# Optimization experiments

Measured on AMD Instinct MI355X. Metric: run time of the kernel, lower is better.

Reference implementation:

```python
import jax, jax.numpy as jnp
import numpy as np

EPS = 1e-5

def _point_batch_norm(x, gamma, beta):
    # BatchNorm1d over channel dim of (B, N, C): stats over (B, N), biased var (training mode)
    mu = jnp.mean(x, axis=(0, 1))
    var = jnp.var(x, axis=(0, 1))
    return (x - mu) * jax.lax.rsqrt(var + EPS) * gamma + beta

def setup_inputs() -> dict:
    key = jax.random.key(0)
    ks = jax.random.split(key, 10)
    B, M, N, K = 4, 16384, 32768, 16
    C, Cs, O = 64, 64, 64
    curr_coords = jax.random.normal(ks[0], (B, M, 3), jnp.float32)
    curr_feat = jax.random.normal(ks[1], (B, M, C), jnp.float32)
    skip_coords = jax.random.normal(ks[2], (B, N, 3), jnp.float32)
    skip_feat = jax.random.normal(ks[3], (B, N, Cs), jnp.float32)
    upsampling_idxs = jax.random.randint(ks[4], (B, N, K), 0, M, jnp.int64)
    s1 = 1.0 / np.sqrt(C)
    s2 = 1.0 / np.sqrt(Cs)
    W1 = jax.random.uniform(ks[5], (C, O), jnp.float32, -s1, s1)
    b1 = jax.random.uniform(ks[6], (O,), jnp.float32, -s1, s1)
    W2 = jax.random.uniform(ks[7], (Cs, O), jnp.float32, -s2, s2)
    b2 = jax.random.uniform(ks[8], (O,), jnp.float32, -s2, s2)
    g1 = jnp.ones((O,), jnp.float32); beta1 = jnp.zeros((O,), jnp.float32)
    g2 = jnp.ones((O,), jnp.float32); beta2 = jnp.zeros((O,), jnp.float32)
    return {
        "curr_coords": curr_coords, "curr_feat": curr_feat,
        "skip_coords": skip_coords, "skip_feat": skip_feat,
        "upsampling_idxs": upsampling_idxs,
        "W1": W1, "b1": b1, "g1": g1, "beta1": beta1,
        "W2": W2, "b2": b2, "g2": g2, "beta2": beta2,
    }

def reference(curr_coords, curr_feat, skip_coords, skip_feat, upsampling_idxs,
              W1, b1, g1, beta1, W2, b2, g2, beta2):
    # Gather K-NN neighbor features per skip point: (B, N, K, C), then max over K
    gathered = jax.vmap(lambda f, i: f[i])(curr_feat, upsampling_idxs)
    pooled = jnp.max(gathered, axis=2)  # (B, N, C)
    # proj: Linear -> PointBatchNorm -> ReLU
    h = jax.nn.relu(_point_batch_norm(pooled @ W1 + b1, g1, beta1))
    # proj_skip on skip features
    hs = jax.nn.relu(_point_batch_norm(skip_feat @ W2 + b2, g2, beta2))
    return jnp.concatenate([skip_coords, h, hs], axis=-1)  # (B, N, 3 + 2*O)
```

## Files before the change

kernel.cpp:

```cpp
#include <hip/hip_runtime.h>
#include <hip/hip_bf16.h>

#define BB 4
#define MM 16384
#define NN 32768
#define KK 16
#define ROWS (BB * NN)
#define OUTW 131
#define RPW 32
#define A_BLOCKS (ROWS / (RPW * 4))

__global__ __launch_bounds__(256) void k_pool_proj(
    const float* __restrict__ cf, const int* __restrict__ idxs,
    const float* __restrict__ scoord,
    const float* __restrict__ W1, const float* __restrict__ b1,
    float* __restrict__ out, float* __restrict__ acc)
{
    __shared__ float pool[4][64];
    __shared__ float lsum[64], lsq[64];
    const int lane = threadIdx.x & 63;
    const int wv   = threadIdx.x >> 6;
    if (threadIdx.x < 64) { lsum[threadIdx.x] = 0.f; lsq[threadIdx.x] = 0.f; }
    __syncthreads();

    const int xcd   = blockIdx.x & 7;
    const int batch = xcd >> 1;
    const int blkIB = ((blockIdx.x >> 3) << 1) | (xcd & 1);
    const int gw    = blkIB * 4 + wv;
    const int rbase = (batch << 15) + gw * RPW;

    float w[64];
#pragma unroll
    for (int c = 0; c < 64; ++c) w[c] = W1[c * 64 + lane];
    const float bias = b1[lane];

    float psum = 0.f, psq = 0.f;
    for (int r0 = 0; r0 < RPW; ++r0) {
        const int r = rbase + r0;
        int mi = 0;
        if (lane < KK) mi = idxs[r * KK + lane];
        float pmax = -3.402823466e38f;
#pragma unroll
        for (int k = 0; k < KK; ++k) {
            const int m = __shfl(mi, k);
            pmax = fmaxf(pmax, cf[(((batch << 14) + m) << 6) + lane]);
        }
        pool[wv][lane] = pmax;
        __builtin_amdgcn_wave_barrier();

        const float4* t4 = (const float4*)(&pool[wv][0]);
        float y = bias;
#pragma unroll
        for (int c4 = 0; c4 < 16; ++c4) {
            const float4 p = t4[c4];
            y = fmaf(p.x, w[c4 * 4 + 0], y);
            y = fmaf(p.y, w[c4 * 4 + 1], y);
            y = fmaf(p.z, w[c4 * 4 + 2], y);
            y = fmaf(p.w, w[c4 * 4 + 3], y);
        }
        __builtin_amdgcn_wave_barrier();

        const size_t ob = (size_t)r * OUTW;
        out[ob + 3 + lane] = y;
        if (lane < 3) out[ob + lane] = scoord[r * 3 + lane];
        psum += y; psq += y * y;
    }
    atomicAdd(&lsum[lane], psum);
    atomicAdd(&lsq[lane], psq);
    __syncthreads();
    if (threadIdx.x < 64) {
        atomicAdd(&acc[threadIdx.x],      lsum[threadIdx.x]);
        atomicAdd(&acc[64 + threadIdx.x], lsq[threadIdx.x]);
    }
}

__global__ __launch_bounds__(256) void k_skip_proj(
    const float* __restrict__ sf,
    const float* __restrict__ W2, const float* __restrict__ b2,
    float* __restrict__ out, float* __restrict__ acc)
{
    __shared__ float srow[4][64];
    __shared__ float lsum[64], lsq[64];
    const int lane = threadIdx.x & 63;
    const int wv   = threadIdx.x >> 6;
    if (threadIdx.x < 64) { lsum[threadIdx.x] = 0.f; lsq[threadIdx.x] = 0.f; }
    __syncthreads();

    float w[64];
#pragma unroll
    for (int c = 0; c < 64; ++c) w[c] = W2[c * 64 + lane];
    const float bias = b2[lane];

    float psum = 0.f, psq = 0.f;
    const int gw = blockIdx.x * 4 + wv;
    for (int r0 = 0; r0 < RPW; ++r0) {
        const int r = gw * RPW + r0;
        srow[wv][lane] = sf[(size_t)r * 64 + lane];
        __builtin_amdgcn_wave_barrier();

        const float4* t4 = (const float4*)(&srow[wv][0]);
        float y = bias;
#pragma unroll
        for (int c4 = 0; c4 < 16; ++c4) {
            const float4 p = t4[c4];
            y = fmaf(p.x, w[c4 * 4 + 0], y);
            y = fmaf(p.y, w[c4 * 4 + 1], y);
            y = fmaf(p.z, w[c4 * 4 + 2], y);
            y = fmaf(p.w, w[c4 * 4 + 3], y);
        }
        __builtin_amdgcn_wave_barrier();

        out[(size_t)r * OUTW + 67 + lane] = y;
        psum += y; psq += y * y;
    }
    atomicAdd(&lsum[lane], psum);
    atomicAdd(&lsq[lane], psq);
    __syncthreads();
    if (threadIdx.x < 64) {
        atomicAdd(&acc[128 + threadIdx.x], lsum[threadIdx.x]);
        atomicAdd(&acc[192 + threadIdx.x], lsq[threadIdx.x]);
    }
}

__global__ void k_stats(float* __restrict__ ws,
                        const float* __restrict__ g1, const float* __restrict__ be1,
                        const float* __restrict__ g2, const float* __restrict__ be2)
{
    const int o = threadIdx.x;
    const float inv = 1.0f / (float)ROWS;
    float m1 = ws[o] * inv;
    float v1 = ws[64 + o] * inv - m1 * m1;
    float a1 = g1[o] * rsqrtf(v1 + 1e-5f);
    ws[256 + o] = a1;
    ws[384 + o] = be1[o] - m1 * a1;
    float m2 = ws[128 + o] * inv;
    float v2 = ws[192 + o] * inv - m2 * m2;
    float a2 = g2[o] * rsqrtf(v2 + 1e-5f);
    ws[256 + 64 + o] = a2;
    ws[384 + 64 + o] = be2[o] - m2 * a2;
}

__global__ __launch_bounds__(256) void k_finalize(float* __restrict__ out,
                                                  const float* __restrict__ ws)
{
    const size_t T  = (size_t)gridDim.x * blockDim.x;
    const size_t t0 = (size_t)blockIdx.x * blockDim.x + threadIdx.x;
#pragma unroll
    for (int i = 0; i < 4; ++i) {
        const size_t e = t0 + (size_t)i * T;
        const size_t r = e >> 7;
        const int    j = (int)(e & 127);
        const size_t ad = r * OUTW + 3 + j;
        const float v = out[ad];
        out[ad] = fmaxf(fmaf(v, ws[256 + j], ws[384 + j]), 0.f);
    }
}

extern "C" void kernel_launch(void* const* d_in, const int* in_sizes, int n_in,
                              void* d_out, int out_size, void* d_ws, size_t ws_size,
                              hipStream_t stream)
{
    const float* cf     = (const float*)d_in[1];
    const float* scoord = (const float*)d_in[2];
    const float* sf     = (const float*)d_in[3];
    const int*   idxs   = (const int*)  d_in[4];
    const float* W1     = (const float*)d_in[5];
    const float* b1     = (const float*)d_in[6];
    const float* g1     = (const float*)d_in[7];
    const float* be1    = (const float*)d_in[8];
    const float* W2     = (const float*)d_in[9];
    const float* b2     = (const float*)d_in[10];
    const float* g2     = (const float*)d_in[11];
    const float* be2    = (const float*)d_in[12];
    float* out = (float*)d_out;
    float* ws  = (float*)d_ws;

    hipMemsetAsync(ws, 0, 256 * sizeof(float), stream);
    k_pool_proj<<<A_BLOCKS, 256, 0, stream>>>(cf, idxs, scoord, W1, b1, out, ws);
    k_skip_proj<<<A_BLOCKS, 256, 0, stream>>>(sf, W2, b2, out, ws);
    k_stats<<<1, 64, 0, stream>>>(ws, g1, be1, g2, be2);
    k_finalize<<<16384, 256, 0, stream>>>(out, ws);
}
```

Baseline: 293.2 us.

## Shrink rows per wave, spread stat atomics over slots, batch skip-proj rows

```diff
diff --git a/kernel.cpp b/kernel.cpp
--- a/kernel.cpp
+++ b/kernel.cpp
@@ -7,8 +7,11 @@
 #define KK 16
 #define ROWS (BB * NN)
 #define OUTW 131
-#define RPW 32
+#define RPW 8
 #define A_BLOCKS (ROWS / (RPW * 4))
+#define NSLOT 16
+#define NEG_INF -3.402823466e38f
+
 
 __global__ __launch_bounds__(256) void k_pool_proj(
     const float* __restrict__ cf, const int* __restrict__ idxs,
@@ -28,6 +31,7 @@
     const int blkIB = ((blockIdx.x >> 3) << 1) | (xcd & 1);
     const int gw    = blkIB * 4 + wv;
     const int rbase = (batch << 15) + gw * RPW;
+    const float* __restrict__ cfb = cf + ((size_t)batch << 20);
 
     float w[64];
 #pragma unroll
@@ -35,15 +39,16 @@
     const float bias = b1[lane];
 
     float psum = 0.f, psq = 0.f;
+#pragma unroll 1
     for (int r0 = 0; r0 < RPW; ++r0) {
         const int r = rbase + r0;
         int mi = 0;
-        if (lane < KK) mi = idxs[r * KK + lane];
-        float pmax = -3.402823466e38f;
+        if (lane < KK) mi = idxs[(size_t)r * KK + lane];
+        float pmax = NEG_INF;
 #pragma unroll
         for (int k = 0; k < KK; ++k) {
             const int m = __shfl(mi, k);
-            pmax = fmaxf(pmax, cf[(((batch << 14) + m) << 6) + lane]);
+            pmax = fmaxf(pmax, cfb[((size_t)m << 6) + lane]);
         }
         pool[wv][lane] = pmax;
         __builtin_amdgcn_wave_barrier();
@@ -62,15 +67,16 @@
 
         const size_t ob = (size_t)r * OUTW;
         out[ob + 3 + lane] = y;
-        if (lane < 3) out[ob + lane] = scoord[r * 3 + lane];
+        if (lane < 3) out[ob + lane] = scoord[(size_t)r * 3 + lane];
         psum += y; psq += y * y;
     }
     atomicAdd(&lsum[lane], psum);
     atomicAdd(&lsq[lane], psq);
     __syncthreads();
     if (threadIdx.x < 64) {
-        atomicAdd(&acc[threadIdx.x],      lsum[threadIdx.x]);
-        atomicAdd(&acc[64 + threadIdx.x], lsq[threadIdx.x]);
+        float* slot = acc + (blockIdx.x & (NSLOT - 1)) * 256;
+        atomicAdd(&slot[threadIdx.x],      lsum[threadIdx.x]);
+        atomicAdd(&slot[64 + threadIdx.x], lsq[threadIdx.x]);
     }
 }
 
@@ -79,7 +85,7 @@
     const float* __restrict__ W2, const float* __restrict__ b2,
     float* __restrict__ out, float* __restrict__ acc)
 {
-    __shared__ float srow[4][64];
+    __shared__ float tile[4][4][64];
     __shared__ float lsum[64], lsq[64];
     const int lane = threadIdx.x & 63;
     const int wv   = threadIdx.x >> 6;
@@ -90,35 +96,53 @@
 #pragma unroll
     for (int c = 0; c < 64; ++c) w[c] = W2[c * 64 + lane];
     const float bias = b2[lane];
+    const float4* __restrict__ sf4 = (const float4*)sf;
+
+    const int gw    = blockIdx.x * 4 + wv;
+    const int rbase = gw * RPW;
 
     float psum = 0.f, psq = 0.f;
-    const int gw = blockIdx.x * 4 + wv;
-    for (int r0 = 0; r0 < RPW; ++r0) {
-        const int r = gw * RPW + r0;
-        srow[wv][lane] = sf[(size_t)r * 64 + lane];
-        __builtin_amdgcn_wave_barrier();
-
-        const float4* t4 = (const float4*)(&srow[wv][0]);
-        float y = bias;
+#pragma unroll 1
+    for (int it = 0; it < RPW / 4; ++it) {
+        const int r4 = rbase + it * 4;
+        const float4 v = sf4[(size_t)r4 * 16 + lane];
+        ((float4*)&tile[wv][0][0])[lane] = v;
+        __builtin_amdgcn_wave_barrier();
+
+        const float4* t0 = (const float4*)&tile[wv][0][0];
+        const float4* t1 = (const float4*)&tile[wv][1][0];
+        const float4* t2 = (const float4*)&tile[wv][2][0];
+        const float4* t3 = (const float4*)&tile[wv][3][0];
+        float y0 = bias, y1 = bias, y2 = bias, y3 = bias;
 #pragma unroll
         for (int c4 = 0; c4 < 16; ++c4) {
-            const float4 p = t4[c4];
-            y = fmaf(p.x, w[c4 * 4 + 0], y);
-            y = fmaf(p.y, w[c4 * 4 + 1], y);
-            y = fmaf(p.z, w[c4 * 4 + 2], y);
-            y = fmaf(p.w, w[c4 * 4 + 3], y);
+            const float4 p0 = t0[c4], p1 = t1[c4], p2 = t2[c4], p3 = t3[c4];
+            const float wa = w[4*c4+0], wb = w[4*c4+1], wc = w[4*c4+2], wd = w[4*c4+3];
+            y0 = fmaf(p0.x, wa, y0); y0 = fmaf(p0.y, wb, y0);
+            y0 = fmaf(p0.z, wc, y0); y0 = fmaf(p0.w, wd, y0);
+            y1 = fmaf(p1.x, wa, y1); y1 = fmaf(p1.y, wb, y1);
+            y1 = fmaf(p1.z, wc, y1); y1 = fmaf(p1.w, wd, y1);
+            y2 = fmaf(p2.x, wa, y2); y2 = fmaf(p2.y, wb, y2);
+            y2 = fmaf(p2.z, wc, y2); y2 = fmaf(p2.w, wd, y2);
+            y3 = fmaf(p3.x, wa, y3); y3 = fmaf(p3.y, wb, y3);
+            y3 = fmaf(p3.z, wc, y3); y3 = fmaf(p3.w, wd, y3);
         }
         __builtin_amdgcn_wave_barrier();
 
-        out[(size_t)r * OUTW + 67 + lane] = y;
-        psum += y; psq += y * y;
+        out[(size_t)(r4 + 0) * OUTW + 67 + lane] = y0;
+        out[(size_t)(r4 + 1) * OUTW + 67 + lane] = y1;
+        out[(size_t)(r4 + 2) * OUTW + 67 + lane] = y2;
+        out[(size_t)(r4 + 3) * OUTW + 67 + lane] = y3;
+        psum += y0 + y1 + y2 + y3;
+        psq  += y0*y0 + y1*y1 + y2*y2 + y3*y3;
     }
     atomicAdd(&lsum[lane], psum);
     atomicAdd(&lsq[lane], psq);
     __syncthreads();
     if (threadIdx.x < 64) {
-        atomicAdd(&acc[128 + threadIdx.x], lsum[threadIdx.x]);
-        atomicAdd(&acc[192 + threadIdx.x], lsq[threadIdx.x]);
+        float* slot = acc + (blockIdx.x & (NSLOT - 1)) * 256;
+        atomicAdd(&slot[128 + threadIdx.x], lsum[threadIdx.x]);
+        atomicAdd(&slot[192 + threadIdx.x], lsq[threadIdx.x]);
     }
 }
 
@@ -127,32 +151,42 @@
                         const float* __restrict__ g2, const float* __restrict__ be2)
 {
     const int o = threadIdx.x;
+    float s1 = 0.f, q1 = 0.f, s2 = 0.f, q2 = 0.f;
+#pragma unroll
+    for (int s = 0; s < NSLOT; ++s) {
+        const float* p = ws + s * 256;
+        s1 += p[o]; q1 += p[64 + o]; s2 += p[128 + o]; q2 += p[192 + o];
+    }
     const float inv = 1.0f / (float)ROWS;
-    float m1 = ws[o] * inv;
-    float v1 = ws[64 + o] * inv - m1 * m1;
-    float a1 = g1[o] * rsqrtf(v1 + 1e-5f);
-    ws[256 + o] = a1;
-    ws[384 + o] = be1[o] - m1 * a1;
-    float m2 = ws[128 + o] * inv;
-    float v2 = ws[192 + o] * inv - m2 * m2;
-    float a2 = g2[o] * rsqrtf(v2 + 1e-5f);
-    ws[256 + 64 + o] = a2;
-    ws[384 + 64 + o] = be2[o] - m2 * a2;
+    const float m1 = s1 * inv;
+    const float a1 = g1[o] * rsqrtf(q1 * inv - m1 * m1 + 1e-5f);
+    ws[4096 + o] = a1;
+    ws[4224 + o] = be1[o] - m1 * a1;
+    const float m2 = s2 * inv;
+    const float a2 = g2[o] * rsqrtf(q2 * inv - m2 * m2 + 1e-5f);
+    ws[4096 + 64 + o] = a2;
+    ws[4224 + 64 + o] = be2[o] - m2 * a2;
 }
 
 __global__ __launch_bounds__(256) void k_finalize(float* __restrict__ out,
                                                   const float* __restrict__ ws)
 {
+    __shared__ float aN[128], cN[128];
+    const int t = threadIdx.x;
+    if (t < 128)      aN[t] = ws[4096 + t];
+    else              cN[t - 128] = ws[4224 + (t - 128)];
+    __syncthreads();
+
     const size_t T  = (size_t)gridDim.x * blockDim.x;
-    const size_t t0 = (size_t)blockIdx.x * blockDim.x + threadIdx.x;
-#pragma unroll
-    for (int i = 0; i < 4; ++i) {
+    const size_t t0 = (size_t)blockIdx.x * blockDim.x + t;
+#pragma unroll
+    for (int i = 0; i < 8; ++i) {
         const size_t e = t0 + (size_t)i * T;
         const size_t r = e >> 7;
         const int    j = (int)(e & 127);
         const size_t ad = r * OUTW + 3 + j;
         const float v = out[ad];
-        out[ad] = fmaxf(fmaf(v, ws[256 + j], ws[384 + j]), 0.f);
+        out[ad] = fmaxf(fmaf(v, aN[j], cN[j]), 0.f);
     }
 }
 
@@ -175,9 +209,9 @@
     float* out = (float*)d_out;
     float* ws  = (float*)d_ws;
 
-    hipMemsetAsync(ws, 0, 256 * sizeof(float), stream);
+    hipMemsetAsync(ws, 0, NSLOT * 256 * sizeof(float), stream);
     k_pool_proj<<<A_BLOCKS, 256, 0, stream>>>(cf, idxs, scoord, W1, b1, out, ws);
     k_skip_proj<<<A_BLOCKS, 256, 0, stream>>>(sf, W2, b2, out, ws);
     k_stats<<<1, 64, 0, stream>>>(ws, g1, be1, g2, be2);
-    k_finalize<<<16384, 256, 0, stream>>>(out, ws);
-}
+    k_finalize<<<8192, 256, 0, stream>>>(out, ws);
+}
```

Result: no change. 296.0 us (+0.9%).
